# Performance work log

Measured on AMD Instinct MI355X. Metric: run time of the kernel, lower is better.

## Reference

```python
import jax, jax.numpy as jnp
import numpy as np

T, B, H, L = 200, 32, 1024, 2
DROPOUT = 0.32
KEEP = 1.0 - DROPOUT
FORGET_GATE_BIAS = 1.0


def setup_inputs() -> dict:
    key = jax.random.key(0)
    ks = jax.random.split(key, 8)
    scale = 1.0 / np.sqrt(H)  # torch LSTM default init: U(-1/sqrt(H), 1/sqrt(H))
    x = jax.random.normal(ks[0], (T, B, H), jnp.float32)
    W_ih = jax.random.uniform(ks[1], (L, 4 * H, H), jnp.float32, -scale, scale)
    W_hh = jax.random.uniform(ks[2], (L, 4 * H, H), jnp.float32, -scale, scale)
    b_ih = jax.random.uniform(ks[3], (L, 4 * H), jnp.float32, -scale, scale)
    b_hh = jax.random.uniform(ks[4], (L, 4 * H), jnp.float32, -scale, scale)
    # forget-gate bias init as in LstmDrop.__init__ (gate order i,f,g,o)
    b_ih = b_ih.at[:, H:2 * H].set(FORGET_GATE_BIAS)
    b_hh = b_hh.at[:, H:2 * H].set(0.0)
    h0 = jnp.zeros((L, B, H), jnp.float32)
    c0 = jnp.zeros((L, B, H), jnp.float32)
    # inverted dropout masks: inter-layer (torch LSTM dropout, applied to all but last layer)
    # and the trailing inplace Dropout on the output sequence
    mask_inter = (jax.random.bernoulli(ks[5], KEEP, (L - 1, T, B, H)) / KEEP).astype(jnp.float32)
    mask_out = (jax.random.bernoulli(ks[6], KEEP, (T, B, H)) / KEEP).astype(jnp.float32)
    return {"x": x, "h0": h0, "c0": c0, "W_ih": W_ih, "W_hh": W_hh,
            "b_ih": b_ih, "b_hh": b_hh, "mask_inter": mask_inter, "mask_out": mask_out}


def _lstm_layer(xs, h, c, Wih, Whh, b):
    # xs: [T,B,in]; Wih/Whh: [4H,in]/[4H,H]; b: [4H] (b_ih + b_hh fused)
    def step(carry, x_t):
        h, c = carry
        gates = x_t @ Wih.T + h @ Whh.T + b  # [B,4H]
        i, f, g, o = jnp.split(gates, 4, axis=-1)
        c = jax.nn.sigmoid(f) * c + jax.nn.sigmoid(i) * jnp.tanh(g)
        h = jax.nn.sigmoid(o) * jnp.tanh(c)
        return (h, c), h
    (hT, cT), ys = jax.lax.scan(step, (h, c), xs)
    return ys, hT, cT


def reference(x, h0, c0, W_ih, W_hh, b_ih, b_hh, mask_inter, mask_out):
    y = x
    h_last, c_last = [], []
    for l in range(L):
        y, hT, cT = _lstm_layer(y, h0[l], c0[l], W_ih[l], W_hh[l], b_ih[l] + b_hh[l])
        h_last.append(hT)
        c_last.append(cT)
        if l < L - 1:  # torch LSTM applies dropout between layers only
            y = y * mask_inter[l]
    y = y * mask_out  # the inplace Dropout on the output sequence
    return y, jnp.stack(h_last), jnp.stack(c_last)
```

## Files before the change

kernel.cpp:

```cpp
#include <hip/hip_runtime.h>

#define T_STEPS 200
#define BATCH   32
#define HID     1024
#define NWG     256
#define NTHR    512

typedef _Float16 half8 __attribute__((ext_vector_type(8)));
typedef float    f32x4 __attribute__((ext_vector_type(4)));

struct Bar {
    unsigned flag[NWG * 32];
    unsigned gen[8 * 32];
};

__device__ __forceinline__ half8 ld_coh16(const _Float16* p) {
    union { unsigned long long u[2]; half8 h; } r;
    const unsigned long long* q = (const unsigned long long*)p;
    r.u[0] = __hip_atomic_load(q,     __ATOMIC_RELAXED, __HIP_MEMORY_SCOPE_AGENT);
    r.u[1] = __hip_atomic_load(q + 1, __ATOMIC_RELAXED, __HIP_MEMORY_SCOPE_AGENT);
    return r.h;
}
__device__ __forceinline__ void st_coh16(_Float16* p, half8 v) {
    union { half8 h; unsigned long long u[2]; } r; r.h = v;
    unsigned long long* q = (unsigned long long*)p;
    __hip_atomic_store(q,     r.u[0], __ATOMIC_RELAXED, __HIP_MEMORY_SCOPE_AGENT);
    __hip_atomic_store(q + 1, r.u[1], __ATOMIC_RELAXED, __HIP_MEMORY_SCOPE_AGENT);
}

__device__ __forceinline__ half8 cvt8(const float* p) {
    f32x4 lo = *(const f32x4*)p;
    f32x4 hi = *(const f32x4*)(p + 4);
    half8 a;
    a[0] = (_Float16)lo[0]; a[1] = (_Float16)lo[1];
    a[2] = (_Float16)lo[2]; a[3] = (_Float16)lo[3];
    a[4] = (_Float16)hi[0]; a[5] = (_Float16)hi[1];
    a[6] = (_Float16)hi[2]; a[7] = (_Float16)hi[3];
    return a;
}

__global__ void init_k(const float* __restrict__ h0,
                       _Float16* __restrict__ h0b, _Float16* __restrict__ h1b,
                       Bar* __restrict__ bar) {
    int i = blockIdx.x * blockDim.x + threadIdx.x;
    if (i < BATCH * HID) {
        h0b[i] = (_Float16)h0[i];
        h1b[i] = (_Float16)h0[BATCH * HID + i];
    }
    if (blockIdx.x == 0) {
        if (threadIdx.x < NWG) bar->flag[threadIdx.x * 32] = 0;
        if (threadIdx.x < 8)   bar->gen[threadIdx.x * 32]  = 0;
    }
}

__global__ __launch_bounds__(NTHR, 2) void lstm_main(
    const float* __restrict__ x, const float* __restrict__ c0,
    const float* __restrict__ Wih, const float* __restrict__ Whh,
    const float* __restrict__ bih, const float* __restrict__ bhh,
    const float* __restrict__ mi, const float* __restrict__ mo,
    float* __restrict__ out,
    _Float16* __restrict__ y0m, _Float16* __restrict__ h0b,
    _Float16* __restrict__ h1b, Bar* __restrict__ bar)
{
    __shared__ _Float16 W_s[32 * 2048];
    __shared__ float scr[8][2][16][17];
    __shared__ float c_s[BATCH][8];
    __shared__ alignas(16) _Float16 st_h[BATCH][8];
    __shared__ alignas(16) _Float16 st_y[BATCH][8];

    const int bid   = blockIdx.x;
    const int layer = bid >> 7;
    const int wgl   = bid & 127;
    const int tid   = threadIdx.x;

    const float* WihL = Wih + (size_t)layer * 4 * HID * HID;
    const float* WhhL = Whh + (size_t)layer * 4 * HID * HID;
    for (int idx = tid; idx < 32 * 2048; idx += NTHR) {
        int r = idx >> 11, k = idx & 2047;
        int grow = (r >> 3) * HID + wgl * 8 + (r & 7);
        float v = (k < HID) ? WihL[(size_t)grow * HID + k]
                            : WhhL[(size_t)grow * HID + (k - HID)];
        W_s[idx ^ ((r & 7) << 3)] = (_Float16)v;
    }

    float bias0 = 0.f, bias1 = 0.f, bias2 = 0.f, bias3 = 0.f;
    int b_ = 0, col_ = 0, gcol = 0;
    if (tid < 256) {
        b_ = tid >> 3; col_ = tid & 7; gcol = wgl * 8 + col_;
        bias0 = bih[layer * 4096 + gcol]           + bhh[layer * 4096 + gcol];
        bias1 = bih[layer * 4096 + HID + gcol]     + bhh[layer * 4096 + HID + gcol];
        bias2 = bih[layer * 4096 + 2 * HID + gcol] + bhh[layer * 4096 + 2 * HID + gcol];
        bias3 = bih[layer * 4096 + 3 * HID + gcol] + bhh[layer * 4096 + 3 * HID + gcol];
        c_s[b_][col_] = c0[((size_t)layer * BATCH + b_) * HID + gcol];
    }
    __syncthreads();

    const int lane = tid & 63, wid = tid >> 6;
    const int m  = wid & 1;
    const int kq = wid >> 1;
    const int row = lane & 15, bb = m * 16 + row, ko = (lane >> 4) * 8;
    const int grp = bid & 7;

    half8 aF[16];
    float mi_reg = 0.f, mo_reg = 0.f;
    if (layer == 0) {
        if (kq < 2) {
            const float* xp = x + (size_t)bb * HID + kq * 512 + ko;
            #pragma unroll
            for (int kk = 0; kk < 16; ++kk) aF[kk] = cvt8(xp + kk * 32);
        }
        if (tid < 256) mi_reg = mi[(size_t)b_ * HID + gcol];
    }

    for (int tk = 0; tk <= T_STEPS; ++tk) {
        const bool active = (layer == 0) ? (tk < T_STEPS) : (tk >= 1);
        if (active) {
            const int t = (layer == 0) ? tk : tk - 1;
            if (layer == 0) {
                if (kq >= 2) {
                    const _Float16* hp = h0b + (tk & 1) * (BATCH * HID)
                                       + bb * HID + (kq - 2) * 512 + ko;
                    #pragma unroll
                    for (int kk = 0; kk < 16; ++kk) aF[kk] = ld_coh16(hp + kk * 32);
                }
            } else {
                if (kq < 2) {
                    const _Float16* yp = y0m + ((size_t)t * BATCH + bb) * HID + kq * 512 + ko;
                    #pragma unroll
                    for (int kk = 0; kk < 16; ++kk) aF[kk] = ld_coh16(yp + kk * 32);
                } else {
                    const _Float16* hp = h1b + (((tk + 1) & 1)) * (BATCH * HID)
                                       + bb * HID + (kq - 2) * 512 + ko;
                    #pragma unroll
                    for (int kk = 0; kk < 16; ++kk) aF[kk] = ld_coh16(hp + kk * 32);
                }
            }

            f32x4 acc0 = {0.f, 0.f, 0.f, 0.f}, acc1 = {0.f, 0.f, 0.f, 0.f};
            #pragma unroll
            for (int kk = 0; kk < 16; ++kk) {
                const int k  = kq * 512 + kk * 32 + ko;
                const int r1 = 16 + row;
                const half8 b0 = *(const half8*)&W_s[(row * 2048 + k) ^ ((row & 7) << 3)];
                const half8 b1 = *(const half8*)&W_s[(r1 * 2048 + k) ^ ((r1 & 7) << 3)];
                acc0 = __builtin_amdgcn_mfma_f32_16x16x32_f16(aF[kk], b0, acc0, 0, 0, 0);
                acc1 = __builtin_amdgcn_mfma_f32_16x16x32_f16(aF[kk], b1, acc1, 0, 0, 0);
            }
            #pragma unroll
            for (int j = 0; j < 4; ++j) {
                scr[wid][0][(lane >> 4) * 4 + j][row] = acc0[j];
                scr[wid][1][(lane >> 4) * 4 + j][row] = acc1[j];
            }
            __syncthreads();

            if (tid < 256) {
                const int m2 = b_ >> 4, rD = b_ & 15;
                float v0 = 0.f, v1 = 0.f, v2 = 0.f, v3 = 0.f;
                #pragma unroll
                for (int q = 0; q < 4; ++q) {
                    v0 += scr[q * 2 + m2][0][rD][col_];
                    v1 += scr[q * 2 + m2][0][rD][8 + col_];
                    v2 += scr[q * 2 + m2][1][rD][col_];
                    v3 += scr[q * 2 + m2][1][rD][8 + col_];
                }
                const float ig = 1.f / (1.f + __expf(-(v0 + bias0)));
                const float fg = 1.f / (1.f + __expf(-(v1 + bias1)));
                const float gg = tanhf(v2 + bias2);
                const float og = 1.f / (1.f + __expf(-(v3 + bias3)));
                const float cc = fg * c_s[b_][col_] + ig * gg;
                const float hh = og * tanhf(cc);
                c_s[b_][col_] = cc;

                st_h[b_][col_] = (_Float16)hh;

                const size_t oidx = ((size_t)t * BATCH + b_) * HID + gcol;
                if (layer == 0) {
                    st_y[b_][col_] = (_Float16)(hh * mi_reg);
                } else {
                    out[oidx] = hh * mo_reg;
                }
                if (t == T_STEPS - 1) {
                    const size_t base = (size_t)T_STEPS * BATCH * HID;
                    out[base + ((size_t)layer * BATCH + b_) * HID + gcol] = hh;
                    out[base + (size_t)2 * BATCH * HID + ((size_t)layer * BATCH + b_) * HID + gcol] = cc;
                }
            }
            __syncthreads();

            if (tid < BATCH) {
                _Float16* hwr = (layer == 0) ? (h0b + (((tk + 1) & 1)) * (BATCH * HID))
                                             : (h1b + ((tk & 1)) * (BATCH * HID));
                st_coh16(&hwr[tid * HID + wgl * 8], *(const half8*)st_h[tid]);
                if (layer == 0)
                    st_coh16(&y0m[((size_t)t * BATCH + tid) * HID + wgl * 8],
                             *(const half8*)st_y[tid]);
            }
        }

        if (tk == T_STEPS) break;

        const unsigned tgt = (unsigned)(tk + 1);

        if (tid == 0) {
            asm volatile("s_waitcnt vmcnt(0)" ::: "memory");
            __hip_atomic_store(&bar->flag[bid * 32], tgt,
                               __ATOMIC_RELAXED, __HIP_MEMORY_SCOPE_AGENT);
        }

        if (layer == 0) {
            if (kq < 2 && tk + 1 < T_STEPS) {
                const float* xp = x + ((size_t)(tk + 1) * BATCH + bb) * HID + kq * 512 + ko;
                #pragma unroll
                for (int kk = 0; kk < 16; ++kk) aF[kk] = cvt8(xp + kk * 32);
            }
            if (tid < 256 && tk + 1 < T_STEPS)
                mi_reg = mi[((size_t)(tk + 1) * BATCH + b_) * HID + gcol];
        } else {
            if (tid < 256 && tk < T_STEPS)
                mo_reg = mo[((size_t)tk * BATCH + b_) * HID + gcol];
        }

        if (bid == 0) {
            if (tid < NWG) {
                while (__hip_atomic_load(&bar->flag[tid * 32], __ATOMIC_RELAXED,
                                         __HIP_MEMORY_SCOPE_AGENT) < tgt)
                    __builtin_amdgcn_s_sleep(1);
            }
            __syncthreads();
            if (tid < 8)
                __hip_atomic_store(&bar->gen[tid * 32], tgt,
                                   __ATOMIC_RELAXED, __HIP_MEMORY_SCOPE_AGENT);
        } else {
            if (tid == 0) {
                while (__hip_atomic_load(&bar->gen[grp * 32], __ATOMIC_RELAXED,
                                         __HIP_MEMORY_SCOPE_AGENT) < tgt)
                    __builtin_amdgcn_s_sleep(1);
            }
        }
        asm volatile("" ::: "memory");
        __syncthreads();
    }
}

extern "C" void kernel_launch(void* const* d_in, const int* in_sizes, int n_in,
                              void* d_out, int out_size, void* d_ws, size_t ws_size,
                              hipStream_t stream) {
    const float* x   = (const float*)d_in[0];
    const float* h0  = (const float*)d_in[1];
    const float* c0  = (const float*)d_in[2];
    const float* Wih = (const float*)d_in[3];
    const float* Whh = (const float*)d_in[4];
    const float* bih = (const float*)d_in[5];
    const float* bhh = (const float*)d_in[6];
    const float* mi  = (const float*)d_in[7];
    const float* mo  = (const float*)d_in[8];
    float* out = (float*)d_out;

    char* w = (char*)d_ws;
    _Float16* y0m = (_Float16*)w;
    _Float16* h0b = (_Float16*)(w + 13107200);
    _Float16* h1b = (_Float16*)(w + 13107200 + 131072);
    Bar*      bar = (Bar*)(w + 13107200 + 262144);

    hipLaunchKernelGGL(init_k, dim3(128), dim3(256), 0, stream, h0, h0b, h1b, bar);

    void* args[] = {(void*)&x, (void*)&c0, (void*)&Wih, (void*)&Whh,
                    (void*)&bih, (void*)&bhh, (void*)&mi, (void*)&mo,
                    (void*)&out, (void*)&y0m, (void*)&h0b, (void*)&h1b, (void*)&bar};
    hipLaunchCooperativeKernel((void*)lstm_main, dim3(NWG), dim3(NTHR),
                               args, 0, stream);
}
```

Baseline: 2.452 ms.

## Replace centralized grid barrier with per-layer flag dataflow waits

Drops the two-level global barrier (one master block gathering all flags, then broadcasting a generation counter). Each block now polls only the per-block flags it actually depends on: layer-0 blocks wait on layer-0 flags, layer-1 blocks wait on layer-0 progress and on layer-1 flags. This lets the two layers run as a loosely coupled pipeline and removes a global round trip per step. Wave roles are also remapped so the publishing and prefetch waves (x loads, mask loads, h/y stores, output writes) do their work off the critical path after the gate computation. The spin loops busy-wait without sleeping, which adds polling traffic, and the correctness of the ordering depends on relaxed atomics plus waitcnt.

```diff
diff --git a/kernel.cpp b/kernel.cpp
--- a/kernel.cpp
+++ b/kernel.cpp
@@ -8,11 +8,6 @@
 
 typedef _Float16 half8 __attribute__((ext_vector_type(8)));
 typedef float    f32x4 __attribute__((ext_vector_type(4)));
-
-struct Bar {
-    unsigned flag[NWG * 32];
-    unsigned gen[8 * 32];
-};
 
 __device__ __forceinline__ half8 ld_coh16(const _Float16* p) {
     union { unsigned long long u[2]; half8 h; } r;
@@ -41,15 +36,15 @@
 
 __global__ void init_k(const float* __restrict__ h0,
                        _Float16* __restrict__ h0b, _Float16* __restrict__ h1b,
-                       Bar* __restrict__ bar) {
+                       unsigned* __restrict__ flag0, unsigned* __restrict__ flag1) {
     int i = blockIdx.x * blockDim.x + threadIdx.x;
     if (i < BATCH * HID) {
         h0b[i] = (_Float16)h0[i];
         h1b[i] = (_Float16)h0[BATCH * HID + i];
     }
     if (blockIdx.x == 0) {
-        if (threadIdx.x < NWG) bar->flag[threadIdx.x * 32] = 0;
-        if (threadIdx.x < 8)   bar->gen[threadIdx.x * 32]  = 0;
+        if (threadIdx.x < 128)      flag0[threadIdx.x * 32] = 0;
+        else if (threadIdx.x < 256) flag1[(threadIdx.x - 128) * 32] = 0;
     }
 }
 
@@ -60,13 +55,15 @@
     const float* __restrict__ mi, const float* __restrict__ mo,
     float* __restrict__ out,
     _Float16* __restrict__ y0m, _Float16* __restrict__ h0b,
-    _Float16* __restrict__ h1b, Bar* __restrict__ bar)
+    _Float16* __restrict__ h1b, unsigned* __restrict__ flag0,
+    unsigned* __restrict__ flag1)
 {
     __shared__ _Float16 W_s[32 * 2048];
     __shared__ float scr[8][2][16][17];
     __shared__ float c_s[BATCH][8];
     __shared__ alignas(16) _Float16 st_h[BATCH][8];
     __shared__ alignas(16) _Float16 st_y[BATCH][8];
+    __shared__ float st_o[BATCH][8];
 
     const int bid   = blockIdx.x;
     const int layer = bid >> 7;
@@ -93,152 +90,157 @@
         bias3 = bih[layer * 4096 + 3 * HID + gcol] + bhh[layer * 4096 + 3 * HID + gcol];
         c_s[b_][col_] = c0[((size_t)layer * BATCH + b_) * HID + gcol];
     }
+    const int ot = tid - 256;
+    const int b2 = (ot >= 0) ? (ot >> 3) : 0, c2 = (ot >= 0) ? (ot & 7) : 0;
+    const int gcol2 = wgl * 8 + c2;
     __syncthreads();
 
     const int lane = tid & 63, wid = tid >> 6;
-    const int m  = wid & 1;
-    const int kq = wid >> 1;
-    const int row = lane & 15, bb = m * 16 + row, ko = (lane >> 4) * 8;
-    const int grp = bid & 7;
+    int kq;
+    if (layer == 0) kq = (wid < 4) ? (2 + (wid >> 1)) : ((wid - 4) >> 1);
+    else            kq = wid >> 1;
+    const int mm   = wid & 1;
+    const int srow = kq * 2 + mm;
+    const int row = lane & 15, bb = mm * 16 + row, ko = (lane >> 4) * 8;
 
     half8 aF[16];
     float mi_reg = 0.f, mo_reg = 0.f;
-    if (layer == 0) {
-        if (kq < 2) {
-            const float* xp = x + (size_t)bb * HID + kq * 512 + ko;
-            #pragma unroll
-            for (int kk = 0; kk < 16; ++kk) aF[kk] = cvt8(xp + kk * 32);
-        }
-        if (tid < 256) mi_reg = mi[(size_t)b_ * HID + gcol];
-    }
-
-    for (int tk = 0; tk <= T_STEPS; ++tk) {
-        const bool active = (layer == 0) ? (tk < T_STEPS) : (tk >= 1);
-        if (active) {
-            const int t = (layer == 0) ? tk : tk - 1;
-            if (layer == 0) {
-                if (kq >= 2) {
-                    const _Float16* hp = h0b + (tk & 1) * (BATCH * HID)
-                                       + bb * HID + (kq - 2) * 512 + ko;
-                    #pragma unroll
-                    for (int kk = 0; kk < 16; ++kk) aF[kk] = ld_coh16(hp + kk * 32);
-                }
-            } else {
-                if (kq < 2) {
-                    const _Float16* yp = y0m + ((size_t)t * BATCH + bb) * HID + kq * 512 + ko;
-                    #pragma unroll
-                    for (int kk = 0; kk < 16; ++kk) aF[kk] = ld_coh16(yp + kk * 32);
-                } else {
-                    const _Float16* hp = h1b + (((tk + 1) & 1)) * (BATCH * HID)
-                                       + bb * HID + (kq - 2) * 512 + ko;
-                    #pragma unroll
-                    for (int kk = 0; kk < 16; ++kk) aF[kk] = ld_coh16(hp + kk * 32);
-                }
-            }
-
-            f32x4 acc0 = {0.f, 0.f, 0.f, 0.f}, acc1 = {0.f, 0.f, 0.f, 0.f};
-            #pragma unroll
-            for (int kk = 0; kk < 16; ++kk) {
-                const int k  = kq * 512 + kk * 32 + ko;
-                const int r1 = 16 + row;
-                const half8 b0 = *(const half8*)&W_s[(row * 2048 + k) ^ ((row & 7) << 3)];
-                const half8 b1 = *(const half8*)&W_s[(r1 * 2048 + k) ^ ((r1 & 7) << 3)];
-                acc0 = __builtin_amdgcn_mfma_f32_16x16x32_f16(aF[kk], b0, acc0, 0, 0, 0);
-                acc1 = __builtin_amdgcn_mfma_f32_16x16x32_f16(aF[kk], b1, acc1, 0, 0, 0);
-            }
-            #pragma unroll
-            for (int j = 0; j < 4; ++j) {
-                scr[wid][0][(lane >> 4) * 4 + j][row] = acc0[j];
-                scr[wid][1][(lane >> 4) * 4 + j][row] = acc1[j];
-            }
-            __syncthreads();
-
-            if (tid < 256) {
-                const int m2 = b_ >> 4, rD = b_ & 15;
-                float v0 = 0.f, v1 = 0.f, v2 = 0.f, v3 = 0.f;
-                #pragma unroll
-                for (int q = 0; q < 4; ++q) {
-                    v0 += scr[q * 2 + m2][0][rD][col_];
-                    v1 += scr[q * 2 + m2][0][rD][8 + col_];
-                    v2 += scr[q * 2 + m2][1][rD][col_];
-                    v3 += scr[q * 2 + m2][1][rD][8 + col_];
-                }
-                const float ig = 1.f / (1.f + __expf(-(v0 + bias0)));
-                const float fg = 1.f / (1.f + __expf(-(v1 + bias1)));
-                const float gg = tanhf(v2 + bias2);
-                const float og = 1.f / (1.f + __expf(-(v3 + bias3)));
-                const float cc = fg * c_s[b_][col_] + ig * gg;
-                const float hh = og * tanhf(cc);
-                c_s[b_][col_] = cc;
-
-                st_h[b_][col_] = (_Float16)hh;
-
-                const size_t oidx = ((size_t)t * BATCH + b_) * HID + gcol;
-                if (layer == 0) {
-                    st_y[b_][col_] = (_Float16)(hh * mi_reg);
-                } else {
-                    out[oidx] = hh * mo_reg;
-                }
-                if (t == T_STEPS - 1) {
-                    const size_t base = (size_t)T_STEPS * BATCH * HID;
-                    out[base + ((size_t)layer * BATCH + b_) * HID + gcol] = hh;
-                    out[base + (size_t)2 * BATCH * HID + ((size_t)layer * BATCH + b_) * HID + gcol] = cc;
-                }
-            }
-            __syncthreads();
-
-            if (tid < BATCH) {
-                _Float16* hwr = (layer == 0) ? (h0b + (((tk + 1) & 1)) * (BATCH * HID))
-                                             : (h1b + ((tk & 1)) * (BATCH * HID));
-                st_coh16(&hwr[tid * HID + wgl * 8], *(const half8*)st_h[tid]);
-                if (layer == 0)
-                    st_coh16(&y0m[((size_t)t * BATCH + tid) * HID + wgl * 8],
-                             *(const half8*)st_y[tid]);
-            }
-        }
-
-        if (tk == T_STEPS) break;
-
-        const unsigned tgt = (unsigned)(tk + 1);
-
-        if (tid == 0) {
-            asm volatile("s_waitcnt vmcnt(0)" ::: "memory");
-            __hip_atomic_store(&bar->flag[bid * 32], tgt,
-                               __ATOMIC_RELAXED, __HIP_MEMORY_SCOPE_AGENT);
-        }
-
+    if (layer == 0 && kq < 2) {
+        const float* xp = x + (size_t)bb * HID + kq * 512 + ko;
+        #pragma unroll
+        for (int kk = 0; kk < 16; ++kk) aF[kk] = cvt8(xp + kk * 32);
+    }
+    if (layer == 1 && ot >= 0) mo_reg = mo[(size_t)b2 * HID + gcol2];
+
+    for (int s = 0; s < T_STEPS; ++s) {
         if (layer == 0) {
-            if (kq < 2 && tk + 1 < T_STEPS) {
-                const float* xp = x + ((size_t)(tk + 1) * BATCH + bb) * HID + kq * 512 + ko;
-                #pragma unroll
-                for (int kk = 0; kk < 16; ++kk) aF[kk] = cvt8(xp + kk * 32);
-            }
-            if (tid < 256 && tk + 1 < T_STEPS)
-                mi_reg = mi[((size_t)(tk + 1) * BATCH + b_) * HID + gcol];
+            if (tid < 128) {
+                const unsigned* f = flag0 + tid * 32;
+                const unsigned tgt = (unsigned)s;
+                while (__hip_atomic_load(f, __ATOMIC_RELAXED,
+                                         __HIP_MEMORY_SCOPE_AGENT) < tgt) {}
+            }
         } else {
-            if (tid < 256 && tk < T_STEPS)
-                mo_reg = mo[((size_t)tk * BATCH + b_) * HID + gcol];
-        }
-
-        if (bid == 0) {
-            if (tid < NWG) {
-                while (__hip_atomic_load(&bar->flag[tid * 32], __ATOMIC_RELAXED,
-                                         __HIP_MEMORY_SCOPE_AGENT) < tgt)
-                    __builtin_amdgcn_s_sleep(1);
-            }
-            __syncthreads();
-            if (tid < 8)
-                __hip_atomic_store(&bar->gen[tid * 32], tgt,
-                                   __ATOMIC_RELAXED, __HIP_MEMORY_SCOPE_AGENT);
-        } else {
-            if (tid == 0) {
-                while (__hip_atomic_load(&bar->gen[grp * 32], __ATOMIC_RELAXED,
-                                         __HIP_MEMORY_SCOPE_AGENT) < tgt)
-                    __builtin_amdgcn_s_sleep(1);
+            if (tid < 128) {
+                const unsigned* f = flag0 + tid * 32;
+                const unsigned tgt = (unsigned)(s + 1);
+                while (__hip_atomic_load(f, __ATOMIC_RELAXED,
+                                         __HIP_MEMORY_SCOPE_AGENT) < tgt) {}
+            } else if (tid < 256) {
+                const unsigned* f = flag1 + (tid - 128) * 32;
+                const unsigned tgt = (unsigned)s;
+                while (__hip_atomic_load(f, __ATOMIC_RELAXED,
+                                         __HIP_MEMORY_SCOPE_AGENT) < tgt) {}
             }
         }
         asm volatile("" ::: "memory");
         __syncthreads();
+
+        if (layer == 0 && tid < 256)
+            mi_reg = mi[((size_t)s * BATCH + b_) * HID + gcol];
+
+        if (layer == 0) {
+            if (kq >= 2) {
+                const _Float16* hp = h0b + (s & 1) * (BATCH * HID)
+                                   + bb * HID + (kq - 2) * 512 + ko;
+                #pragma unroll
+                for (int kk = 0; kk < 16; ++kk) aF[kk] = ld_coh16(hp + kk * 32);
+            }
+        } else {
+            if (kq < 2) {
+                const _Float16* yp = y0m + ((size_t)s * BATCH + bb) * HID + kq * 512 + ko;
+                #pragma unroll
+                for (int kk = 0; kk < 16; ++kk) aF[kk] = ld_coh16(yp + kk * 32);
+            } else {
+                const _Float16* hp = h1b + (s & 1) * (BATCH * HID)
+                                   + bb * HID + (kq - 2) * 512 + ko;
+                #pragma unroll
+                for (int kk = 0; kk < 16; ++kk) aF[kk] = ld_coh16(hp + kk * 32);
+            }
+        }
+
+        f32x4 acc0 = {0.f, 0.f, 0.f, 0.f}, acc1 = {0.f, 0.f, 0.f, 0.f};
+        #pragma unroll
+        for (int kk = 0; kk < 16; ++kk) {
+            const int k  = kq * 512 + kk * 32 + ko;
+            const int r1 = 16 + row;
+            const half8 bB0 = *(const half8*)&W_s[(row * 2048 + k) ^ ((row & 7) << 3)];
+            const half8 bB1 = *(const half8*)&W_s[(r1 * 2048 + k) ^ ((r1 & 7) << 3)];
+            acc0 = __builtin_amdgcn_mfma_f32_16x16x32_f16(aF[kk], bB0, acc0, 0, 0, 0);
+            acc1 = __builtin_amdgcn_mfma_f32_16x16x32_f16(aF[kk], bB1, acc1, 0, 0, 0);
+        }
+        #pragma unroll
+        for (int j = 0; j < 4; ++j) {
+            scr[srow][0][(lane >> 4) * 4 + j][row] = acc0[j];
+            scr[srow][1][(lane >> 4) * 4 + j][row] = acc1[j];
+        }
+        __syncthreads();
+
+        if (tid < 256) {
+            const int m2 = b_ >> 4, rD = b_ & 15;
+            float v0 = 0.f, v1 = 0.f, v2 = 0.f, v3 = 0.f;
+            #pragma unroll
+            for (int q = 0; q < 4; ++q) {
+                v0 += scr[q * 2 + m2][0][rD][col_];
+                v1 += scr[q * 2 + m2][0][rD][8 + col_];
+                v2 += scr[q * 2 + m2][1][rD][col_];
+                v3 += scr[q * 2 + m2][1][rD][8 + col_];
+            }
+            const float ig = 1.f / (1.f + __expf(-(v0 + bias0)));
+            const float fg = 1.f / (1.f + __expf(-(v1 + bias1)));
+            const float gg = tanhf(v2 + bias2);
+            const float og = 1.f / (1.f + __expf(-(v3 + bias3)));
+            const float cc = fg * c_s[b_][col_] + ig * gg;
+            const float hh = og * tanhf(cc);
+            c_s[b_][col_] = cc;
+
+            st_h[b_][col_] = (_Float16)hh;
+            if (layer == 0) st_y[b_][col_] = (_Float16)(hh * mi_reg);
+            else            st_o[b_][col_] = hh;
+
+            if (s == T_STEPS - 1) {
+                const size_t base = (size_t)T_STEPS * BATCH * HID;
+                out[base + ((size_t)layer * BATCH + b_) * HID + gcol] = hh;
+                out[base + (size_t)2 * BATCH * HID + ((size_t)layer * BATCH + b_) * HID + gcol] = cc;
+            }
+        }
+        __syncthreads();
+
+        if (layer == 0) {
+            if (wid >= 4) {
+                if (tid >= 448 && tid < 480) {
+                    const int sl = tid - 448;
+                    st_coh16(&h0b[((s + 1) & 1) * (BATCH * HID) + sl * HID + wgl * 8],
+                             *(const half8*)st_h[sl]);
+                    st_coh16(&y0m[((size_t)s * BATCH + sl) * HID + wgl * 8],
+                             *(const half8*)st_y[sl]);
+                    asm volatile("s_waitcnt vmcnt(0)" ::: "memory");
+                    if (tid == 448)
+                        __hip_atomic_store(flag0 + wgl * 32, (unsigned)(s + 1),
+                                           __ATOMIC_RELAXED, __HIP_MEMORY_SCOPE_AGENT);
+                }
+                if (kq < 2 && s + 1 < T_STEPS) {
+                    const float* xp = x + ((size_t)(s + 1) * BATCH + bb) * HID + kq * 512 + ko;
+                    #pragma unroll
+                    for (int kk = 0; kk < 16; ++kk) aF[kk] = cvt8(xp + kk * 32);
+                }
+            }
+        } else {
+            if (ot >= 0) {
+                out[((size_t)s * BATCH + b2) * HID + gcol2] = st_o[b2][c2] * mo_reg;
+                if (tid >= 448 && tid < 480) {
+                    const int sl = tid - 448;
+                    st_coh16(&h1b[((s + 1) & 1) * (BATCH * HID) + sl * HID + wgl * 8],
+                             *(const half8*)st_h[sl]);
+                    asm volatile("s_waitcnt vmcnt(0)" ::: "memory");
+                    if (tid == 448)
+                        __hip_atomic_store(flag1 + wgl * 32, (unsigned)(s + 1),
+                                           __ATOMIC_RELAXED, __HIP_MEMORY_SCOPE_AGENT);
+                }
+                if (s + 1 < T_STEPS)
+                    mo_reg = mo[((size_t)(s + 1) * BATCH + b2) * HID + gcol2];
+            }
+        }
     }
 }
 
@@ -257,16 +259,19 @@
     float* out = (float*)d_out;
 
     char* w = (char*)d_ws;
-    _Float16* y0m = (_Float16*)w;
-    _Float16* h0b = (_Float16*)(w + 13107200);
-    _Float16* h1b = (_Float16*)(w + 13107200 + 131072);
-    Bar*      bar = (Bar*)(w + 13107200 + 262144);
-
-    hipLaunchKernelGGL(init_k, dim3(128), dim3(256), 0, stream, h0, h0b, h1b, bar);
+    _Float16* y0m   = (_Float16*)w;
+    _Float16* h0b   = (_Float16*)(w + 13107200);
+    _Float16* h1b   = (_Float16*)(w + 13107200 + 131072);
+    unsigned* flag0 = (unsigned*)(w + 13107200 + 262144);
+    unsigned* flag1 = (unsigned*)(w + 13107200 + 262144 + 16384);
+
+    hipLaunchKernelGGL(init_k, dim3(128), dim3(256), 0, stream,
+                       h0, h0b, h1b, flag0, flag1);
 
     void* args[] = {(void*)&x, (void*)&c0, (void*)&Wih, (void*)&Whh,
                     (void*)&bih, (void*)&bhh, (void*)&mi, (void*)&mo,
-                    (void*)&out, (void*)&y0m, (void*)&h0b, (void*)&h1b, (void*)&bar};
+                    (void*)&out, (void*)&y0m, (void*)&h0b, (void*)&h1b,
+                    (void*)&flag0, (void*)&flag1};
     hipLaunchCooperativeKernel((void*)lstm_main, dim3(NWG), dim3(NTHR),
                                args, 0, stream);
 }
```

Measured after the change: 2.170 ms. 11.5% less time.
